# Optimization experiments

Hardware: AMD Instinct MI355X
Metric: run time of the kernel (lower is better)

The kernel has to match this reference:

```python
import jax, jax.numpy as jnp
import numpy as np

HEADS = 8
LN_EPS = 1e-5


def _elu_plus_one(t):
    # F.elu(x) + 1 == exp(x) for x<0, x+1 for x>=0
    return jax.nn.elu(t) + 1.0


def setup_inputs() -> dict:
    key = jax.random.key(0)
    k1, k2, k3 = jax.random.split(key, 3)
    dim = 256
    x = jax.random.normal(k1, (16, dim, 64, 64), dtype=jnp.float32)
    w_qkv = jax.random.normal(k2, (3 * dim, dim), dtype=jnp.float32) * 0.02
    w_out = jax.random.normal(k3, (dim, dim), dtype=jnp.float32) * 0.02
    ln_gamma = jnp.ones((dim,), dtype=jnp.float32)
    ln_beta = jnp.zeros((dim,), dtype=jnp.float32)
    return {"x": x, "w_qkv": w_qkv, "w_out": w_out, "ln_gamma": ln_gamma, "ln_beta": ln_beta}


def reference(x, w_qkv, w_out, ln_gamma, ln_beta):
    b, c, h, w = x.shape
    hd = c // HEADS
    n = h * w
    # 1x1 conv == per-pixel matmul over channels
    qkv = jnp.einsum('bchw,oc->bohw', x, w_qkv)  # [b, 3c, h, w]
    q, k, v = jnp.split(qkv, 3, axis=1)
    q = q.reshape(b, HEADS, hd, n)
    k = k.reshape(b, HEADS, hd, n)
    v = v.reshape(b, HEADS, hd, n)
    qk = _elu_plus_one(q)
    kk = _elu_plus_one(k)
    # channel-wise kv reduction over spatial positions (NOT an outer product)
    kv = jnp.sum(kk * v, axis=-1, keepdims=True)        # [b, heads, hd, 1]
    denom = jnp.maximum(jnp.sum(kk, axis=-1, keepdims=True), 1e-6)
    out = qk * (kv / denom)                              # [b, heads, hd, n]
    out = out.reshape(b, c, h, w)
    out = jnp.einsum('bchw,oc->bohw', out, w_out)        # 1x1 output conv
    # LayerNorm over channel dim (module permutes to NHWC first)
    t = jnp.transpose(out, (0, 2, 3, 1))                 # [b, h, w, c]
    mu = jnp.mean(t, axis=-1, keepdims=True)
    var = jnp.mean(jnp.square(t - mu), axis=-1, keepdims=True)
    t = (t - mu) * jax.lax.rsqrt(var + LN_EPS) * ln_gamma + ln_beta
    return jnp.transpose(t, (0, 3, 1, 2))
```

## Files before the change

kernel.cpp:

```cpp
#include <hip/hip_runtime.h>


#define NB 16
#define NC 256
#define NN 4096
#define LN_EPS 1e-5f
#define IOSCALE (1.0f/1024.0f)

typedef _Float16 f16;
typedef _Float16 f16x8 __attribute__((ext_vector_type(8)));
typedef _Float16 f16x4v __attribute__((ext_vector_type(4)));
typedef float f32x4 __attribute__((ext_vector_type(4)));

typedef __attribute__((address_space(1))) const unsigned int* as1cu32;
typedef __attribute__((address_space(3))) unsigned int* as3u32;

__device__ __forceinline__ void gload16(const void* g, void* l) {
  __builtin_amdgcn_global_load_lds((as1cu32)g, (as3u32)l, 16, 0, 0);
}
__device__ __forceinline__ float elu1(float x) {
  return x > 0.f ? x + 1.f : __expf(x);
}
#define MFMA16 __builtin_amdgcn_mfma_f32_16x16x32_f16

__global__ __launch_bounds__(256) void k_init(const float* __restrict__ wqkv,
                                              const float* __restrict__ wout,
                                              f16* __restrict__ wh,
                                              f16* __restrict__ wouth,
                                              float* __restrict__ kvden) {
  int i = blockIdx.x * 256 + threadIdx.x;
  wh[i] = (f16)wqkv[i];
  if (i < 65536) wouth[i] = (f16)wout[i];
  if (i < 8192) kvden[i] = 0.f;
}

__global__ __launch_bounds__(256) void k_transpose(const float* __restrict__ x,
                                                   f16* __restrict__ xh) {
  __shared__ float t[64 * 65];
  const int b = blockIdx.z, c0 = blockIdx.y * 64, n0 = blockIdx.x * 64;
  const int tid = threadIdx.x;
#pragma unroll
  for (int i = 0; i < 4; ++i) {
    int lin = tid + i * 256;
    int r = lin >> 4;
    int cg = lin & 15;
    const float4 v = *reinterpret_cast<const float4*>(
        &x[((size_t)(b * NC + c0 + r)) * NN + n0 + cg * 4]);
    t[r * 65 + cg * 4 + 0] = v.x;
    t[r * 65 + cg * 4 + 1] = v.y;
    t[r * 65 + cg * 4 + 2] = v.z;
    t[r * 65 + cg * 4 + 3] = v.w;
  }
  __syncthreads();
#pragma unroll
  for (int i = 0; i < 4; ++i) {
    int lin = tid + i * 256;
    int nr = lin >> 4;
    int cg = lin & 15;
    f16x4v h;
    h[0] = (f16)t[(cg * 4 + 0) * 65 + nr];
    h[1] = (f16)t[(cg * 4 + 1) * 65 + nr];
    h[2] = (f16)t[(cg * 4 + 2) * 65 + nr];
    h[3] = (f16)t[(cg * 4 + 3) * 65 + nr];
    *reinterpret_cast<f16x4v*>(&xh[((size_t)(b * NN + n0 + nr)) * NC + c0 + cg * 4]) = h;
  }
}

__global__ __launch_bounds__(512, 4) void k_kv(const f16* __restrict__ xh,
                                               const f16* __restrict__ wh,
                                               float* __restrict__ kv,
                                               float* __restrict__ den) {
  __shared__ __align__(16) f16 Xc[2][64 * 32];
  __shared__ __align__(16) f16 Bt[2][512 * 32];
  const int b = blockIdx.y;
  const int n0 = blockIdx.x * 64;
  const int tid = threadIdx.x;
  const int lane = tid & 63;
  const int wv = tid >> 6;
  const int ng = wv >> 2, cg = wv & 3;
  const int l15 = lane & 15, lg = lane >> 4;
  const int srow = lane >> 2;
  const int scol = (((lane & 3) ^ (srow & 3)) * 8);
  const int xu = ((lg ^ (l15 & 3)) << 3);

  f32x4 kacc[2][4] = {};
  f32x4 vacc[2][4] = {};

#pragma unroll
  for (int i = 0; i < 4; ++i) {
    const int inst = wv * 4 + i;
    gload16(wh + (size_t)(256 + inst * 16 + srow) * NC + scol, &Bt[0][inst * 512]);
  }
  if (wv < 4)
    gload16(xh + ((size_t)(b * NN + n0 + wv * 16 + srow)) * NC + scol, &Xc[0][wv * 512]);
  __syncthreads();

  for (int s = 0; s < 8; ++s) {
    const int cb = s & 1, nb = (s + 1) & 1;
    if (s < 7) {
      const int c0 = (s + 1) * 32;
#pragma unroll
      for (int i = 0; i < 4; ++i) {
        const int inst = wv * 4 + i;
        gload16(wh + (size_t)(256 + inst * 16 + srow) * NC + c0 + scol, &Bt[nb][inst * 512]);
      }
      if (wv < 4)
        gload16(xh + ((size_t)(b * NN + n0 + wv * 16 + srow)) * NC + c0 + scol, &Xc[nb][wv * 512]);
    }
    const f16x8 a0 = *(const f16x8*)(&Xc[cb][(ng * 32 + l15) * 32 + xu]);
    const f16x8 a1 = *(const f16x8*)(&Xc[cb][(ng * 32 + 16 + l15) * 32 + xu]);
#pragma unroll
    for (int f = 0; f < 4; ++f) {
      const f16x8 bk = *(const f16x8*)(&Bt[cb][(cg * 64 + f * 16 + l15) * 32 + xu]);
      kacc[0][f] = MFMA16(a0, bk, kacc[0][f], 0, 0, 0);
      kacc[1][f] = MFMA16(a1, bk, kacc[1][f], 0, 0, 0);
      const f16x8 bv = *(const f16x8*)(&Bt[cb][(256 + cg * 64 + f * 16 + l15) * 32 + xu]);
      vacc[0][f] = MFMA16(a0, bv, vacc[0][f], 0, 0, 0);
      vacc[1][f] = MFMA16(a1, bv, vacc[1][f], 0, 0, 0);
    }
    if (s < 7) __syncthreads();
  }

  float pkv[4] = {0.f, 0.f, 0.f, 0.f}, pden[4] = {0.f, 0.f, 0.f, 0.f};
#pragma unroll
  for (int f = 0; f < 4; ++f)
#pragma unroll
    for (int m = 0; m < 2; ++m)
#pragma unroll
      for (int j = 0; j < 4; ++j) {
        const float kk = elu1(kacc[m][f][j]);
        pkv[f] += kk * vacc[m][f][j];
        pden[f] += kk;
      }
#pragma unroll
  for (int f = 0; f < 4; ++f) {
    pkv[f] += __shfl_xor(pkv[f], 16, 64);
    pkv[f] += __shfl_xor(pkv[f], 32, 64);
    pden[f] += __shfl_xor(pden[f], 16, 64);
    pden[f] += __shfl_xor(pden[f], 32, 64);
  }
  if (lane < 16) {
#pragma unroll
    for (int f = 0; f < 4; ++f) {
      const int c = cg * 64 + f * 16 + lane;
      atomicAdd(&kv[b * NC + c], pkv[f]);
      atomicAdd(&den[b * NC + c], pden[f]);
    }
  }
}

__global__ __launch_bounds__(512, 4) void k_fused2(const f16* __restrict__ xh,
                                                   const f16* __restrict__ wh,
                                                   const f16* __restrict__ wouth,
                                                   const float* __restrict__ kv,
                                                   const float* __restrict__ den,
                                                   const float* __restrict__ gamma,
                                                   const float* __restrict__ beta,
                                                   float* __restrict__ out) {
  __shared__ __align__(16) f16 Xc[2][64 * 32];
  __shared__ __align__(16) f16 Wt[2][256 * 32];
  __shared__ __align__(16) f16 Q[64 * 256];
  const int b = blockIdx.y;
  const int n0 = blockIdx.x * 64;
  const int tid = threadIdx.x;
  const int lane = tid & 63;
  const int wv = tid >> 6;
  const int cg = wv >> 1, ng = wv & 1;
  const int l15 = lane & 15, lg = lane >> 4;
  const int srow = lane >> 2;
  const int scol = (((lane & 3) ^ (srow & 3)) * 8);
  const int xu = ((lg ^ (l15 & 3)) << 3);

  float sreg[4][4];
#pragma unroll
  for (int m = 0; m < 4; ++m)
#pragma unroll
    for (int j = 0; j < 4; ++j) {
      const int c = cg * 64 + m * 16 + lg * 4 + j;
      sreg[m][j] = kv[b * NC + c] / fmaxf(den[b * NC + c], 1e-6f) * 1024.0f;
    }

#pragma unroll
  for (int i = 0; i < 2; ++i) {
    const int inst = wv * 2 + i;
    gload16(wh + (size_t)(inst * 16 + srow) * NC + scol, &Wt[0][inst * 512]);
  }
  if (wv < 4)
    gload16(xh + ((size_t)(b * NN + n0 + wv * 16 + srow)) * NC + scol, &Xc[0][wv * 512]);
  __syncthreads();

  f32x4 acc[4][2] = {};
  for (int s = 0; s < 8; ++s) {
    const int cb = s & 1, nb = (s + 1) & 1;
    if (s < 7) {
      const int c0 = (s + 1) * 32;
#pragma unroll
      for (int i = 0; i < 2; ++i) {
        const int inst = wv * 2 + i;
        gload16(wh + (size_t)(inst * 16 + srow) * NC + c0 + scol, &Wt[nb][inst * 512]);
      }
      if (wv < 4)
        gload16(xh + ((size_t)(b * NN + n0 + wv * 16 + srow)) * NC + c0 + scol, &Xc[nb][wv * 512]);
    } else {
#pragma unroll
      for (int i = 0; i < 2; ++i) {
        const int inst = wv * 2 + i;
        gload16(wouth + (size_t)(inst * 16 + srow) * NC + scol, &Wt[nb][inst * 512]);
      }
    }
    f16x8 a[4], bx[2];
#pragma unroll
    for (int m = 0; m < 4; ++m)
      a[m] = *(const f16x8*)(&Wt[cb][(cg * 64 + m * 16 + l15) * 32 + xu]);
#pragma unroll
    for (int f = 0; f < 2; ++f)
      bx[f] = *(const f16x8*)(&Xc[cb][(ng * 32 + f * 16 + l15) * 32 + xu]);
#pragma unroll
    for (int m = 0; m < 4; ++m)
#pragma unroll
      for (int f = 0; f < 2; ++f)
        acc[m][f] = MFMA16(a[m], bx[f], acc[m][f], 0, 0, 0);
    if (s < 7) __syncthreads();
  }

#pragma unroll
  for (int m = 0; m < 4; ++m) {
#pragma unroll
    for (int f = 0; f < 2; ++f) {
      const int n = ng * 32 + f * 16 + l15;
      const int ch = cg * 64 + m * 16 + lg * 4;
      const int u = ch >> 3;
      f16x4v h;
#pragma unroll
      for (int j = 0; j < 4; ++j)
        h[j] = (f16)(elu1(acc[m][f][j]) * sreg[m][j]);
      *reinterpret_cast<f16x4v*>(&Q[n * 256 + ((u ^ (n & 7)) << 3) + (ch & 7)]) = h;
    }
  }
  __syncthreads();

  f32x4 acc2[4][2] = {};
  for (int s = 0; s < 8; ++s) {
    const int cb = s & 1, nb = (s + 1) & 1;
    if (s < 7) {
      const int c0 = (s + 1) * 32;
#pragma unroll
      for (int i = 0; i < 2; ++i) {
        const int inst = wv * 2 + i;
        gload16(wouth + (size_t)(inst * 16 + srow) * NC + c0 + scol, &Wt[nb][inst * 512]);
      }
    }
    f16x8 a[4], bq[2];
#pragma unroll
    for (int m = 0; m < 4; ++m)
      a[m] = *(const f16x8*)(&Wt[cb][(cg * 64 + m * 16 + l15) * 32 + xu]);
#pragma unroll
    for (int f = 0; f < 2; ++f) {
      const int n = ng * 32 + f * 16 + l15;
      const int U = s * 4 + lg;
      bq[f] = *(const f16x8*)(&Q[n * 256 + ((U ^ (n & 7)) << 3)]);
    }
#pragma unroll
    for (int m = 0; m < 4; ++m)
#pragma unroll
      for (int f = 0; f < 2; ++f)
        acc2[m][f] = MFMA16(a[m], bq[f], acc2[m][f], 0, 0, 0);
    if (s < 7) __syncthreads();
  }

  float* red1 = (float*)(&Xc[0][0]);
  float* red2 = red1 + 256;
  float* smu = red2 + 256;
  float* srs = smu + 64;
  float s1[2] = {0, 0}, s2[2] = {0, 0};
#pragma unroll
  for (int f = 0; f < 2; ++f)
#pragma unroll
    for (int m = 0; m < 4; ++m)
#pragma unroll
      for (int j = 0; j < 4; ++j) {
        const float v = acc2[m][f][j];
        s1[f] += v;
        s2[f] += v * v;
      }
#pragma unroll
  for (int f = 0; f < 2; ++f) {
    s1[f] += __shfl_xor(s1[f], 16, 64);
    s1[f] += __shfl_xor(s1[f], 32, 64);
    s2[f] += __shfl_xor(s2[f], 16, 64);
    s2[f] += __shfl_xor(s2[f], 32, 64);
  }
  __syncthreads();
  if (lane < 16) {
#pragma unroll
    for (int f = 0; f < 2; ++f) {
      red1[cg * 64 + ng * 32 + f * 16 + lane] = s1[f];
      red2[cg * 64 + ng * 32 + f * 16 + lane] = s2[f];
    }
  }
  __syncthreads();
  if (tid < 64) {
    const float a1 = red1[tid] + red1[64 + tid] + red1[128 + tid] + red1[192 + tid];
    const float a2 = red2[tid] + red2[64 + tid] + red2[128 + tid] + red2[192 + tid];
    const float mu = a1 * (IOSCALE / 256.f);
    const float e2 = a2 * (IOSCALE * IOSCALE / 256.f);
    smu[tid] = mu;
    srs[tid] = rsqrtf(e2 - mu * mu + LN_EPS);
  }
  __syncthreads();
#pragma unroll
  for (int m = 0; m < 4; ++m) {
    const int ob = cg * 64 + m * 16 + lg * 4;
#pragma unroll
    for (int j = 0; j < 4; ++j) {
      const int o = ob + j;
      const float g = gamma[o], be = beta[o];
#pragma unroll
      for (int f = 0; f < 2; ++f) {
        const int col = ng * 32 + f * 16 + l15;
        const float v = acc2[m][f][j] * IOSCALE;
        out[((size_t)(b * NC + o)) * NN + n0 + col] = (v - smu[col]) * srs[col] * g + be;
      }
    }
  }
}

extern "C" void kernel_launch(void* const* d_in, const int* in_sizes, int n_in,
                              void* d_out, int out_size, void* d_ws, size_t ws_size,
                              hipStream_t stream) {
  const float* x = (const float*)d_in[0];
  const float* w_qkv = (const float*)d_in[1];
  const float* w_out = (const float*)d_in[2];
  const float* ln_g = (const float*)d_in[3];
  const float* ln_b = (const float*)d_in[4];
  float* out = (float*)d_out;

  char* wsb = (char*)d_ws;
  const size_t OFF_WH = 0;
  const size_t OFF_WOUTH = 393216;
  const size_t OFF_XH = OFF_WOUTH + 131072;
  const size_t OFF_KV = OFF_XH + 33554432;
  const size_t OFF_DEN = OFF_KV + 16384;

  f16* wh = (f16*)(wsb + OFF_WH);
  f16* wouth = (f16*)(wsb + OFF_WOUTH);
  f16* xh = (f16*)(wsb + OFF_XH);
  float* kv = (float*)(wsb + OFF_KV);
  float* den = (float*)(wsb + OFF_DEN);

  k_init<<<768, 256, 0, stream>>>(w_qkv, w_out, wh, wouth, kv);
  k_transpose<<<dim3(64, 4, 16), 256, 0, stream>>>(x, xh);
  k_kv<<<dim3(64, 16), 512, 0, stream>>>(xh, wh, kv, den);
  k_fused2<<<dim3(64, 16), 512, 0, stream>>>(xh, wh, wouth, kv, den, ln_g, ln_b, out);
}
```

Baseline: 94.43 us.

## Triple-buffer fused kernel loads, double spatial tile, use raw barriers and waitcnts

Restructures k_fused2 so each block handles 128 spatial positions instead of 64, halving the grid and doubling per-wave MFMA work and weight reuse. Global-to-LDS staging moves from double to triple buffering, with manual vmcnt waits, raw s_barrier and setprio around the MFMA bursts, so loads overlap compute with fewer full syncs. The kv/den scale is computed once into shared memory. In exchange the kernel needs much more LDS and more registers, lowering occupancy to about one block per CU, and the manual waitcnt counting is fragile.

```diff
diff --git a/kernel.cpp b/kernel.cpp
--- a/kernel.cpp
+++ b/kernel.cpp
@@ -22,6 +22,25 @@
   return x > 0.f ? x + 1.f : __expf(x);
 }
 #define MFMA16 __builtin_amdgcn_mfma_f32_16x16x32_f16
+
+#define FENCE() asm volatile("" ::: "memory")
+#define SBAR()                                  \
+  do {                                          \
+    FENCE();                                    \
+    __builtin_amdgcn_sched_barrier(0);          \
+    __builtin_amdgcn_s_barrier();               \
+    __builtin_amdgcn_sched_barrier(0);          \
+    FENCE();                                    \
+  } while (0)
+
+template <int N> __device__ __forceinline__ void waitv() {
+  if constexpr (N == 0) asm volatile("s_waitcnt vmcnt(0)" ::: "memory");
+  else if constexpr (N == 2) asm volatile("s_waitcnt vmcnt(2)" ::: "memory");
+  else asm volatile("s_waitcnt vmcnt(3)" ::: "memory");
+}
+__device__ __forceinline__ void waitl0() {
+  asm volatile("s_waitcnt lgkmcnt(0)" ::: "memory");
+}
 
 __global__ __launch_bounds__(256) void k_init(const float* __restrict__ wqkv,
                                               const float* __restrict__ wout,
@@ -149,7 +168,7 @@
   }
 }
 
-__global__ __launch_bounds__(512, 4) void k_fused2(const f16* __restrict__ xh,
+__global__ __launch_bounds__(512, 1) void k_fused2(const f16* __restrict__ xh,
                                                    const f16* __restrict__ wh,
                                                    const f16* __restrict__ wouth,
                                                    const float* __restrict__ kv,
@@ -157,11 +176,12 @@
                                                    const float* __restrict__ gamma,
                                                    const float* __restrict__ beta,
                                                    float* __restrict__ out) {
-  __shared__ __align__(16) f16 Xc[2][64 * 32];
-  __shared__ __align__(16) f16 Wt[2][256 * 32];
-  __shared__ __align__(16) f16 Q[64 * 256];
+  __shared__ __align__(16) f16 Wt[3 * 256 * 32];
+  __shared__ __align__(16) f16 Xc[3 * 128 * 32];
+  __shared__ __align__(16) f16 Q[128 * 256];
+  __shared__ float s1024[256];
   const int b = blockIdx.y;
-  const int n0 = blockIdx.x * 64;
+  const int n0 = blockIdx.x * 128;
   const int tid = threadIdx.x;
   const int lane = tid & 63;
   const int wv = tid >> 6;
@@ -171,110 +191,114 @@
   const int scol = (((lane & 3) ^ (srow & 3)) * 8);
   const int xu = ((lg ^ (l15 & 3)) << 3);
 
-  float sreg[4][4];
-#pragma unroll
-  for (int m = 0; m < 4; ++m)
-#pragma unroll
-    for (int j = 0; j < 4; ++j) {
-      const int c = cg * 64 + m * 16 + lg * 4 + j;
-      sreg[m][j] = kv[b * NC + c] / fmaxf(den[b * NC + c], 1e-6f) * 1024.0f;
-    }
-
-#pragma unroll
-  for (int i = 0; i < 2; ++i) {
-    const int inst = wv * 2 + i;
-    gload16(wh + (size_t)(inst * 16 + srow) * NC + scol, &Wt[0][inst * 512]);
-  }
-  if (wv < 4)
-    gload16(xh + ((size_t)(b * NN + n0 + wv * 16 + srow)) * NC + scol, &Xc[0][wv * 512]);
-  __syncthreads();
-
-  f32x4 acc[4][2] = {};
+  if (tid < 256)
+    s1024[tid] = kv[b * NC + tid] / fmaxf(den[b * NC + tid], 1e-6f) * 1024.0f;
+  waitv<0>();
+
+  auto stageC = [&](int c, int buf) {
+    const int c0 = c * 32;
+    gload16(xh + ((size_t)(b * NN + n0 + wv * 16 + srow)) * NC + c0 + scol,
+            &Xc[buf * 4096 + wv * 512]);
+    gload16(wh + (size_t)(wv * 32 + srow) * NC + c0 + scol,
+            &Wt[buf * 8192 + wv * 1024]);
+    gload16(wh + (size_t)(wv * 32 + 16 + srow) * NC + c0 + scol,
+            &Wt[buf * 8192 + wv * 1024 + 512]);
+  };
+  auto stageW = [&](int c, int buf) {
+    const int c0 = c * 32;
+    gload16(wouth + (size_t)(wv * 32 + srow) * NC + c0 + scol,
+            &Wt[buf * 8192 + wv * 1024]);
+    gload16(wouth + (size_t)(wv * 32 + 16 + srow) * NC + c0 + scol,
+            &Wt[buf * 8192 + wv * 1024 + 512]);
+  };
+
+  stageC(0, 0);
+  stageC(1, 1);
+  waitv<3>();
+  waitl0();
+  SBAR();
+
+  f32x4 acc[4][4] = {};
   for (int s = 0; s < 8; ++s) {
-    const int cb = s & 1, nb = (s + 1) & 1;
-    if (s < 7) {
-      const int c0 = (s + 1) * 32;
-#pragma unroll
-      for (int i = 0; i < 2; ++i) {
-        const int inst = wv * 2 + i;
-        gload16(wh + (size_t)(inst * 16 + srow) * NC + c0 + scol, &Wt[nb][inst * 512]);
-      }
-      if (wv < 4)
-        gload16(xh + ((size_t)(b * NN + n0 + wv * 16 + srow)) * NC + c0 + scol, &Xc[nb][wv * 512]);
-    } else {
-#pragma unroll
-      for (int i = 0; i < 2; ++i) {
-        const int inst = wv * 2 + i;
-        gload16(wouth + (size_t)(inst * 16 + srow) * NC + scol, &Wt[nb][inst * 512]);
-      }
-    }
-    f16x8 a[4], bx[2];
-#pragma unroll
-    for (int m = 0; m < 4; ++m)
-      a[m] = *(const f16x8*)(&Wt[cb][(cg * 64 + m * 16 + l15) * 32 + xu]);
-#pragma unroll
-    for (int f = 0; f < 2; ++f)
-      bx[f] = *(const f16x8*)(&Xc[cb][(ng * 32 + f * 16 + l15) * 32 + xu]);
-#pragma unroll
-    for (int m = 0; m < 4; ++m)
-#pragma unroll
-      for (int f = 0; f < 2; ++f)
-        acc[m][f] = MFMA16(a[m], bx[f], acc[m][f], 0, 0, 0);
-    if (s < 7) __syncthreads();
+    if (s < 6) stageC(s + 2, (s + 2) % 3);
+    else stageW(s - 6, (s + 2) % 3);
+    {
+      const f16* Wb = &Wt[(s % 3) * 8192];
+      const f16* Xb = &Xc[(s % 3) * 4096];
+      f16x8 a[4], bx[4];
+#pragma unroll
+      for (int m = 0; m < 4; ++m)
+        a[m] = *(const f16x8*)(Wb + (cg * 64 + m * 16 + l15) * 32 + xu);
+#pragma unroll
+      for (int f = 0; f < 4; ++f)
+        bx[f] = *(const f16x8*)(Xb + (ng * 64 + f * 16 + l15) * 32 + xu);
+      __builtin_amdgcn_s_setprio(1);
+#pragma unroll
+      for (int m = 0; m < 4; ++m)
+#pragma unroll
+        for (int f = 0; f < 4; ++f)
+          acc[m][f] = MFMA16(a[m], bx[f], acc[m][f], 0, 0, 0);
+      __builtin_amdgcn_s_setprio(0);
+    }
+    if (s < 6) waitv<3>();
+    else waitv<2>();
+    SBAR();
   }
 
 #pragma unroll
   for (int m = 0; m < 4; ++m) {
-#pragma unroll
-    for (int f = 0; f < 2; ++f) {
-      const int n = ng * 32 + f * 16 + l15;
-      const int ch = cg * 64 + m * 16 + lg * 4;
-      const int u = ch >> 3;
+    const int ch = cg * 64 + m * 16 + lg * 4;
+    const float4 sv = *reinterpret_cast<const float4*>(&s1024[ch]);
+    const int u = ch >> 3;
+#pragma unroll
+    for (int f = 0; f < 4; ++f) {
+      const int n = ng * 64 + f * 16 + l15;
       f16x4v h;
-#pragma unroll
-      for (int j = 0; j < 4; ++j)
-        h[j] = (f16)(elu1(acc[m][f][j]) * sreg[m][j]);
+      h[0] = (f16)(elu1(acc[m][f][0]) * sv.x);
+      h[1] = (f16)(elu1(acc[m][f][1]) * sv.y);
+      h[2] = (f16)(elu1(acc[m][f][2]) * sv.z);
+      h[3] = (f16)(elu1(acc[m][f][3]) * sv.w);
       *reinterpret_cast<f16x4v*>(&Q[n * 256 + ((u ^ (n & 7)) << 3) + (ch & 7)]) = h;
     }
   }
-  __syncthreads();
-
-  f32x4 acc2[4][2] = {};
+  waitv<2>();
+  waitl0();
+  SBAR();
+
+  f32x4 acc2[4][4] = {};
   for (int s = 0; s < 8; ++s) {
-    const int cb = s & 1, nb = (s + 1) & 1;
-    if (s < 7) {
-      const int c0 = (s + 1) * 32;
-#pragma unroll
-      for (int i = 0; i < 2; ++i) {
-        const int inst = wv * 2 + i;
-        gload16(wouth + (size_t)(inst * 16 + srow) * NC + c0 + scol, &Wt[nb][inst * 512]);
-      }
-    }
-    f16x8 a[4], bq[2];
-#pragma unroll
-    for (int m = 0; m < 4; ++m)
-      a[m] = *(const f16x8*)(&Wt[cb][(cg * 64 + m * 16 + l15) * 32 + xu]);
-#pragma unroll
-    for (int f = 0; f < 2; ++f) {
-      const int n = ng * 32 + f * 16 + l15;
-      const int U = s * 4 + lg;
-      bq[f] = *(const f16x8*)(&Q[n * 256 + ((U ^ (n & 7)) << 3)]);
-    }
-#pragma unroll
-    for (int m = 0; m < 4; ++m)
-#pragma unroll
-      for (int f = 0; f < 2; ++f)
-        acc2[m][f] = MFMA16(a[m], bq[f], acc2[m][f], 0, 0, 0);
-    if (s < 7) __syncthreads();
-  }
-
-  float* red1 = (float*)(&Xc[0][0]);
-  float* red2 = red1 + 256;
-  float* smu = red2 + 256;
-  float* srs = smu + 64;
-  float s1[2] = {0, 0}, s2[2] = {0, 0};
-#pragma unroll
-  for (int f = 0; f < 2; ++f)
+    if (s < 6) stageW(s + 2, (s + 1) % 3);
+    {
+      const f16* Wb = &Wt[((s + 2) % 3) * 8192];
+      f16x8 a[4], bq[4];
+#pragma unroll
+      for (int m = 0; m < 4; ++m)
+        a[m] = *(const f16x8*)(Wb + (cg * 64 + m * 16 + l15) * 32 + xu);
+#pragma unroll
+      for (int f = 0; f < 4; ++f) {
+        const int n = ng * 64 + f * 16 + l15;
+        const int U = s * 4 + lg;
+        bq[f] = *(const f16x8*)(&Q[n * 256 + ((U ^ (n & 7)) << 3)]);
+      }
+      __builtin_amdgcn_s_setprio(1);
+#pragma unroll
+      for (int m = 0; m < 4; ++m)
+#pragma unroll
+        for (int f = 0; f < 4; ++f)
+          acc2[m][f] = MFMA16(a[m], bq[f], acc2[m][f], 0, 0, 0);
+      __builtin_amdgcn_s_setprio(0);
+    }
+    if (s < 6) { waitv<2>(); SBAR(); }
+    else if (s == 6) { waitv<0>(); SBAR(); }
+  }
+
+  float* red1 = (float*)(&Xc[0]);
+  float* red2 = red1 + 512;
+  float* smu = red2 + 512;
+  float* srs = smu + 128;
+  float s1[4] = {0, 0, 0, 0}, s2[4] = {0, 0, 0, 0};
+#pragma unroll
+  for (int f = 0; f < 4; ++f)
 #pragma unroll
     for (int m = 0; m < 4; ++m)
 #pragma unroll
@@ -284,7 +308,7 @@
         s2[f] += v * v;
       }
 #pragma unroll
-  for (int f = 0; f < 2; ++f) {
+  for (int f = 0; f < 4; ++f) {
     s1[f] += __shfl_xor(s1[f], 16, 64);
     s1[f] += __shfl_xor(s1[f], 32, 64);
     s2[f] += __shfl_xor(s2[f], 16, 64);
@@ -293,15 +317,16 @@
   __syncthreads();
   if (lane < 16) {
 #pragma unroll
-    for (int f = 0; f < 2; ++f) {
-      red1[cg * 64 + ng * 32 + f * 16 + lane] = s1[f];
-      red2[cg * 64 + ng * 32 + f * 16 + lane] = s2[f];
-    }
-  }
-  __syncthreads();
-  if (tid < 64) {
-    const float a1 = red1[tid] + red1[64 + tid] + red1[128 + tid] + red1[192 + tid];
-    const float a2 = red2[tid] + red2[64 + tid] + red2[128 + tid] + red2[192 + tid];
+    for (int f = 0; f < 4; ++f) {
+      const int col = ng * 64 + f * 16 + lane;
+      red1[cg * 128 + col] = s1[f];
+      red2[cg * 128 + col] = s2[f];
+    }
+  }
+  __syncthreads();
+  if (tid < 128) {
+    const float a1 = red1[tid] + red1[128 + tid] + red1[256 + tid] + red1[384 + tid];
+    const float a2 = red2[tid] + red2[128 + tid] + red2[256 + tid] + red2[384 + tid];
     const float mu = a1 * (IOSCALE / 256.f);
     const float e2 = a2 * (IOSCALE * IOSCALE / 256.f);
     smu[tid] = mu;
@@ -316,8 +341,8 @@
       const int o = ob + j;
       const float g = gamma[o], be = beta[o];
 #pragma unroll
-      for (int f = 0; f < 2; ++f) {
-        const int col = ng * 32 + f * 16 + l15;
+      for (int f = 0; f < 4; ++f) {
+        const int col = ng * 64 + f * 16 + l15;
         const float v = acc2[m][f][j] * IOSCALE;
         out[((size_t)(b * NC + o)) * NN + n0 + col] = (v - smu[col]) * srs[col] * g + be;
       }
@@ -351,5 +376,5 @@
   k_init<<<768, 256, 0, stream>>>(w_qkv, w_out, wh, wouth, kv);
   k_transpose<<<dim3(64, 4, 16), 256, 0, stream>>>(x, xh);
   k_kv<<<dim3(64, 16), 512, 0, stream>>>(xh, wh, kv, den);
-  k_fused2<<<dim3(64, 16), 512, 0, stream>>>(xh, wh, wouth, kv, den, ln_g, ln_b, out);
-}
+  k_fused2<<<dim3(32, 16), 512, 0, stream>>>(xh, wh, wouth, kv, den, ln_g, ln_b, out);
+}
```

Result: no change. 94.67 us (+0.3%).

## Stage full X tile in padded LDS and stream weights directly from global

Applied to the files above, without the earlier changes.

Both k_kv and k_fused2 now load the whole 64x256 activation tile into a padded LDS buffer once, then read weight fragments straight from global memory (through cache) into registers instead of double-buffering weight slices through LDS with async global_load_lds. k_kv changes its wave decomposition so that weights are the A operand and pixels the B operand. Its reduction becomes a per-row shuffle across 16 lanes, followed by atomics from more lanes. k_fused2 reuses the X buffer to hold the Q intermediate and drops most per-stage barriers. The intent is to cut synchronisation and LDS traffic, at the cost of exposed global-load latency for weights in the inner loop.

```diff
diff --git a/kernel.cpp b/kernel.cpp
--- a/kernel.cpp
+++ b/kernel.cpp
@@ -12,12 +12,6 @@
 typedef _Float16 f16x4v __attribute__((ext_vector_type(4)));
 typedef float f32x4 __attribute__((ext_vector_type(4)));
 
-typedef __attribute__((address_space(1))) const unsigned int* as1cu32;
-typedef __attribute__((address_space(3))) unsigned int* as3u32;
-
-__device__ __forceinline__ void gload16(const void* g, void* l) {
-  __builtin_amdgcn_global_load_lds((as1cu32)g, (as3u32)l, 16, 0, 0);
-}
 __device__ __forceinline__ float elu1(float x) {
   return x > 0.f ? x + 1.f : __expf(x);
 }
@@ -70,81 +64,67 @@
                                                const f16* __restrict__ wh,
                                                float* __restrict__ kv,
                                                float* __restrict__ den) {
-  __shared__ __align__(16) f16 Xc[2][64 * 32];
-  __shared__ __align__(16) f16 Bt[2][512 * 32];
+  __shared__ __align__(16) f16 Xt[64 * 264];
   const int b = blockIdx.y;
   const int n0 = blockIdx.x * 64;
   const int tid = threadIdx.x;
   const int lane = tid & 63;
   const int wv = tid >> 6;
-  const int ng = wv >> 2, cg = wv & 3;
+  const int cg = wv >> 1, ng = wv & 1;
   const int l15 = lane & 15, lg = lane >> 4;
-  const int srow = lane >> 2;
-  const int scol = (((lane & 3) ^ (srow & 3)) * 8);
-  const int xu = ((lg ^ (l15 & 3)) << 3);
-
-  f32x4 kacc[2][4] = {};
-  f32x4 vacc[2][4] = {};
 
 #pragma unroll
   for (int i = 0; i < 4; ++i) {
-    const int inst = wv * 4 + i;
-    gload16(wh + (size_t)(256 + inst * 16 + srow) * NC + scol, &Bt[0][inst * 512]);
-  }
-  if (wv < 4)
-    gload16(xh + ((size_t)(b * NN + n0 + wv * 16 + srow)) * NC + scol, &Xc[0][wv * 512]);
-  __syncthreads();
-
+    const int idx = i * 512 + tid;
+    const int row = idx >> 5, u = idx & 31;
+    const f16x8 h = *(const f16x8*)(xh + ((size_t)(b * NN + n0 + row)) * NC + u * 8);
+    *reinterpret_cast<f16x8*>(&Xt[row * 264 + u * 8]) = h;
+  }
+  __syncthreads();
+
+  f32x4 kacc[4][2] = {};
+  f32x4 vacc[4][2] = {};
+  const f16* wk = wh + (size_t)(256 + cg * 64 + l15) * NC;
+  const f16* wvp = wh + (size_t)(512 + cg * 64 + l15) * NC;
+#pragma unroll
   for (int s = 0; s < 8; ++s) {
-    const int cb = s & 1, nb = (s + 1) & 1;
-    if (s < 7) {
-      const int c0 = (s + 1) * 32;
-#pragma unroll
-      for (int i = 0; i < 4; ++i) {
-        const int inst = wv * 4 + i;
-        gload16(wh + (size_t)(256 + inst * 16 + srow) * NC + c0 + scol, &Bt[nb][inst * 512]);
-      }
-      if (wv < 4)
-        gload16(xh + ((size_t)(b * NN + n0 + wv * 16 + srow)) * NC + c0 + scol, &Xc[nb][wv * 512]);
-    }
-    const f16x8 a0 = *(const f16x8*)(&Xc[cb][(ng * 32 + l15) * 32 + xu]);
-    const f16x8 a1 = *(const f16x8*)(&Xc[cb][(ng * 32 + 16 + l15) * 32 + xu]);
-#pragma unroll
-    for (int f = 0; f < 4; ++f) {
-      const f16x8 bk = *(const f16x8*)(&Bt[cb][(cg * 64 + f * 16 + l15) * 32 + xu]);
-      kacc[0][f] = MFMA16(a0, bk, kacc[0][f], 0, 0, 0);
-      kacc[1][f] = MFMA16(a1, bk, kacc[1][f], 0, 0, 0);
-      const f16x8 bv = *(const f16x8*)(&Bt[cb][(256 + cg * 64 + f * 16 + l15) * 32 + xu]);
-      vacc[0][f] = MFMA16(a0, bv, vacc[0][f], 0, 0, 0);
-      vacc[1][f] = MFMA16(a1, bv, vacc[1][f], 0, 0, 0);
-    }
-    if (s < 7) __syncthreads();
-  }
-
-  float pkv[4] = {0.f, 0.f, 0.f, 0.f}, pden[4] = {0.f, 0.f, 0.f, 0.f};
-#pragma unroll
-  for (int f = 0; f < 4; ++f)
-#pragma unroll
-    for (int m = 0; m < 2; ++m)
-#pragma unroll
-      for (int j = 0; j < 4; ++j) {
+    const int k0 = s * 32 + lg * 8;
+    f16x8 bx[2];
+#pragma unroll
+    for (int f = 0; f < 2; ++f)
+      bx[f] = *(const f16x8*)(&Xt[(ng * 32 + f * 16 + l15) * 264 + k0]);
+#pragma unroll
+    for (int m = 0; m < 4; ++m) {
+      const f16x8 ak = *(const f16x8*)(wk + (size_t)(m * 16) * NC + k0);
+      const f16x8 av = *(const f16x8*)(wvp + (size_t)(m * 16) * NC + k0);
+#pragma unroll
+      for (int f = 0; f < 2; ++f) {
+        kacc[m][f] = MFMA16(ak, bx[f], kacc[m][f], 0, 0, 0);
+        vacc[m][f] = MFMA16(av, bx[f], vacc[m][f], 0, 0, 0);
+      }
+    }
+  }
+
+#pragma unroll
+  for (int m = 0; m < 4; ++m) {
+#pragma unroll
+    for (int j = 0; j < 4; ++j) {
+      float a = 0.f, d = 0.f;
+#pragma unroll
+      for (int f = 0; f < 2; ++f) {
         const float kk = elu1(kacc[m][f][j]);
-        pkv[f] += kk * vacc[m][f][j];
-        pden[f] += kk;
-      }
-#pragma unroll
-  for (int f = 0; f < 4; ++f) {
-    pkv[f] += __shfl_xor(pkv[f], 16, 64);
-    pkv[f] += __shfl_xor(pkv[f], 32, 64);
-    pden[f] += __shfl_xor(pden[f], 16, 64);
-    pden[f] += __shfl_xor(pden[f], 32, 64);
-  }
-  if (lane < 16) {
-#pragma unroll
-    for (int f = 0; f < 4; ++f) {
-      const int c = cg * 64 + f * 16 + lane;
-      atomicAdd(&kv[b * NC + c], pkv[f]);
-      atomicAdd(&den[b * NC + c], pden[f]);
+        a += kk * vacc[m][f][j];
+        d += kk;
+      }
+      a += __shfl_xor(a, 1, 64);  d += __shfl_xor(d, 1, 64);
+      a += __shfl_xor(a, 2, 64);  d += __shfl_xor(d, 2, 64);
+      a += __shfl_xor(a, 4, 64);  d += __shfl_xor(d, 4, 64);
+      a += __shfl_xor(a, 8, 64);  d += __shfl_xor(d, 8, 64);
+      if (l15 == 0) {
+        const int c = cg * 64 + m * 16 + lg * 4 + j;
+        atomicAdd(&kv[b * NC + c], a);
+        atomicAdd(&den[b * NC + c], d);
+      }
     }
   }
 }
@@ -157,9 +137,9 @@
                                                    const float* __restrict__ gamma,
                                                    const float* __restrict__ beta,
                                                    float* __restrict__ out) {
-  __shared__ __align__(16) f16 Xc[2][64 * 32];
-  __shared__ __align__(16) f16 Wt[2][256 * 32];
-  __shared__ __align__(16) f16 Q[64 * 256];
+  __shared__ __align__(16) f16 XQ[64 * 264];
+  __shared__ float s1024[256];
+  __shared__ float red1[4][64], red2[4][64], smu[64], srs[64];
   const int b = blockIdx.y;
   const int n0 = blockIdx.x * 64;
   const int tid = threadIdx.x;
@@ -167,111 +147,76 @@
   const int wv = tid >> 6;
   const int cg = wv >> 1, ng = wv & 1;
   const int l15 = lane & 15, lg = lane >> 4;
-  const int srow = lane >> 2;
-  const int scol = (((lane & 3) ^ (srow & 3)) * 8);
-  const int xu = ((lg ^ (l15 & 3)) << 3);
-
-  float sreg[4][4];
-#pragma unroll
-  for (int m = 0; m < 4; ++m)
-#pragma unroll
-    for (int j = 0; j < 4; ++j) {
-      const int c = cg * 64 + m * 16 + lg * 4 + j;
-      sreg[m][j] = kv[b * NC + c] / fmaxf(den[b * NC + c], 1e-6f) * 1024.0f;
-    }
-
-#pragma unroll
-  for (int i = 0; i < 2; ++i) {
-    const int inst = wv * 2 + i;
-    gload16(wh + (size_t)(inst * 16 + srow) * NC + scol, &Wt[0][inst * 512]);
-  }
-  if (wv < 4)
-    gload16(xh + ((size_t)(b * NN + n0 + wv * 16 + srow)) * NC + scol, &Xc[0][wv * 512]);
+
+#pragma unroll
+  for (int i = 0; i < 4; ++i) {
+    const int idx = i * 512 + tid;
+    const int row = idx >> 5, u = idx & 31;
+    const f16x8 h = *(const f16x8*)(xh + ((size_t)(b * NN + n0 + row)) * NC + u * 8);
+    *reinterpret_cast<f16x8*>(&XQ[row * 264 + u * 8]) = h;
+  }
+  if (tid < 256)
+    s1024[tid] = kv[b * NC + tid] / fmaxf(den[b * NC + tid], 1e-6f) * 1024.0f;
   __syncthreads();
 
   f32x4 acc[4][2] = {};
-  for (int s = 0; s < 8; ++s) {
-    const int cb = s & 1, nb = (s + 1) & 1;
-    if (s < 7) {
-      const int c0 = (s + 1) * 32;
-#pragma unroll
-      for (int i = 0; i < 2; ++i) {
-        const int inst = wv * 2 + i;
-        gload16(wh + (size_t)(inst * 16 + srow) * NC + c0 + scol, &Wt[nb][inst * 512]);
-      }
-      if (wv < 4)
-        gload16(xh + ((size_t)(b * NN + n0 + wv * 16 + srow)) * NC + c0 + scol, &Xc[nb][wv * 512]);
-    } else {
-#pragma unroll
-      for (int i = 0; i < 2; ++i) {
-        const int inst = wv * 2 + i;
-        gload16(wouth + (size_t)(inst * 16 + srow) * NC + scol, &Wt[nb][inst * 512]);
-      }
-    }
-    f16x8 a[4], bx[2];
-#pragma unroll
-    for (int m = 0; m < 4; ++m)
-      a[m] = *(const f16x8*)(&Wt[cb][(cg * 64 + m * 16 + l15) * 32 + xu]);
-#pragma unroll
-    for (int f = 0; f < 2; ++f)
-      bx[f] = *(const f16x8*)(&Xc[cb][(ng * 32 + f * 16 + l15) * 32 + xu]);
-#pragma unroll
-    for (int m = 0; m < 4; ++m)
+  {
+    const f16* wq = wh + (size_t)(cg * 64 + l15) * NC;
+#pragma unroll
+    for (int s = 0; s < 8; ++s) {
+      const int k0 = s * 32 + lg * 8;
+      f16x8 bx[2];
 #pragma unroll
       for (int f = 0; f < 2; ++f)
-        acc[m][f] = MFMA16(a[m], bx[f], acc[m][f], 0, 0, 0);
-    if (s < 7) __syncthreads();
-  }
+        bx[f] = *(const f16x8*)(&XQ[(ng * 32 + f * 16 + l15) * 264 + k0]);
+#pragma unroll
+      for (int m = 0; m < 4; ++m) {
+        const f16x8 aq = *(const f16x8*)(wq + (size_t)(m * 16) * NC + k0);
+#pragma unroll
+        for (int f = 0; f < 2; ++f)
+          acc[m][f] = MFMA16(aq, bx[f], acc[m][f], 0, 0, 0);
+      }
+    }
+  }
+  __syncthreads();
 
 #pragma unroll
   for (int m = 0; m < 4; ++m) {
+    const int ch = cg * 64 + m * 16 + lg * 4;
+    const float4 sv = *reinterpret_cast<const float4*>(&s1024[ch]);
 #pragma unroll
     for (int f = 0; f < 2; ++f) {
       const int n = ng * 32 + f * 16 + l15;
-      const int ch = cg * 64 + m * 16 + lg * 4;
-      const int u = ch >> 3;
       f16x4v h;
-#pragma unroll
-      for (int j = 0; j < 4; ++j)
-        h[j] = (f16)(elu1(acc[m][f][j]) * sreg[m][j]);
-      *reinterpret_cast<f16x4v*>(&Q[n * 256 + ((u ^ (n & 7)) << 3) + (ch & 7)]) = h;
+      h[0] = (f16)(elu1(acc[m][f][0]) * sv.x);
+      h[1] = (f16)(elu1(acc[m][f][1]) * sv.y);
+      h[2] = (f16)(elu1(acc[m][f][2]) * sv.z);
+      h[3] = (f16)(elu1(acc[m][f][3]) * sv.w);
+      *reinterpret_cast<f16x4v*>(&XQ[n * 264 + ch]) = h;
     }
   }
   __syncthreads();
 
   f32x4 acc2[4][2] = {};
-  for (int s = 0; s < 8; ++s) {
-    const int cb = s & 1, nb = (s + 1) & 1;
-    if (s < 7) {
-      const int c0 = (s + 1) * 32;
-#pragma unroll
-      for (int i = 0; i < 2; ++i) {
-        const int inst = wv * 2 + i;
-        gload16(wouth + (size_t)(inst * 16 + srow) * NC + c0 + scol, &Wt[nb][inst * 512]);
-      }
-    }
-    f16x8 a[4], bq[2];
-#pragma unroll
-    for (int m = 0; m < 4; ++m)
-      a[m] = *(const f16x8*)(&Wt[cb][(cg * 64 + m * 16 + l15) * 32 + xu]);
-#pragma unroll
-    for (int f = 0; f < 2; ++f) {
-      const int n = ng * 32 + f * 16 + l15;
-      const int U = s * 4 + lg;
-      bq[f] = *(const f16x8*)(&Q[n * 256 + ((U ^ (n & 7)) << 3)]);
-    }
-#pragma unroll
-    for (int m = 0; m < 4; ++m)
+  {
+    const f16* wo = wouth + (size_t)(cg * 64 + l15) * NC;
+#pragma unroll
+    for (int s = 0; s < 8; ++s) {
+      const int k0 = s * 32 + lg * 8;
+      f16x8 bq[2];
 #pragma unroll
       for (int f = 0; f < 2; ++f)
-        acc2[m][f] = MFMA16(a[m], bq[f], acc2[m][f], 0, 0, 0);
-    if (s < 7) __syncthreads();
-  }
-
-  float* red1 = (float*)(&Xc[0][0]);
-  float* red2 = red1 + 256;
-  float* smu = red2 + 256;
-  float* srs = smu + 64;
+        bq[f] = *(const f16x8*)(&XQ[(ng * 32 + f * 16 + l15) * 264 + k0]);
+#pragma unroll
+      for (int m = 0; m < 4; ++m) {
+        const f16x8 ao = *(const f16x8*)(wo + (size_t)(m * 16) * NC + k0);
+#pragma unroll
+        for (int f = 0; f < 2; ++f)
+          acc2[m][f] = MFMA16(ao, bq[f], acc2[m][f], 0, 0, 0);
+      }
+    }
+  }
+
   float s1[2] = {0, 0}, s2[2] = {0, 0};
 #pragma unroll
   for (int f = 0; f < 2; ++f)
@@ -290,18 +235,18 @@
     s2[f] += __shfl_xor(s2[f], 16, 64);
     s2[f] += __shfl_xor(s2[f], 32, 64);
   }
-  __syncthreads();
   if (lane < 16) {
 #pragma unroll
     for (int f = 0; f < 2; ++f) {
-      red1[cg * 64 + ng * 32 + f * 16 + lane] = s1[f];
-      red2[cg * 64 + ng * 32 + f * 16 + lane] = s2[f];
+      const int col = ng * 32 + f * 16 + lane;
+      red1[cg][col] = s1[f];
+      red2[cg][col] = s2[f];
     }
   }
   __syncthreads();
   if (tid < 64) {
-    const float a1 = red1[tid] + red1[64 + tid] + red1[128 + tid] + red1[192 + tid];
-    const float a2 = red2[tid] + red2[64 + tid] + red2[128 + tid] + red2[192 + tid];
+    const float a1 = red1[0][tid] + red1[1][tid] + red1[2][tid] + red1[3][tid];
+    const float a2 = red2[0][tid] + red2[1][tid] + red2[2][tid] + red2[3][tid];
     const float mu = a1 * (IOSCALE / 256.f);
     const float e2 = a2 * (IOSCALE * IOSCALE / 256.f);
     smu[tid] = mu;
```

New measurement: 190.0 us. 101% more time.

## Double spatial tile to 128 and stage full X tile in LDS once

Applied to the files above, without the earlier changes.

Both the kv and fused kernels now process 128 spatial positions per 1024-thread block instead of 64 with 512 threads. The whole X tile (128x256 fp16) is loaded into LDS up front instead of being double-buffered per K-step. Only the weight slices stay double-buffered, and the fused kernel reuses the X buffer to hold Q. The goal is to halve how often each block re-reads the weights and to cut per-step global loads. In exchange LDS per block grows to about 96KB, which limits blocks per CU, and the grid is halved to 512 blocks.

```diff
diff --git a/kernel.cpp b/kernel.cpp
--- a/kernel.cpp
+++ b/kernel.cpp
@@ -66,57 +66,71 @@
   }
 }
 
-__global__ __launch_bounds__(512, 4) void k_kv(const f16* __restrict__ xh,
-                                               const f16* __restrict__ wh,
-                                               float* __restrict__ kv,
-                                               float* __restrict__ den) {
-  __shared__ __align__(16) f16 Xc[2][64 * 32];
+__global__ __launch_bounds__(1024, 4) void k_kv(const f16* __restrict__ xh,
+                                                const f16* __restrict__ wh,
+                                                float* __restrict__ kv,
+                                                float* __restrict__ den) {
+  __shared__ __align__(16) f16 Xt[128 * 256];
   __shared__ __align__(16) f16 Bt[2][512 * 32];
   const int b = blockIdx.y;
-  const int n0 = blockIdx.x * 64;
+  const int n0 = blockIdx.x * 128;
   const int tid = threadIdx.x;
   const int lane = tid & 63;
   const int wv = tid >> 6;
   const int ng = wv >> 2, cg = wv & 3;
   const int l15 = lane & 15, lg = lane >> 4;
-  const int srow = lane >> 2;
-  const int scol = (((lane & 3) ^ (srow & 3)) * 8);
-  const int xu = ((lg ^ (l15 & 3)) << 3);
+
+  {
+    const int rsub = lane >> 5;
+    const int u = lane & 31;
+#pragma unroll
+    for (int i = 0; i < 4; ++i) {
+      const int inst = wv * 4 + i;
+      const int row = inst * 2 + rsub;
+      gload16(xh + ((size_t)(b * NN + n0 + row)) * NC + ((u ^ (row & 31)) * 8),
+              &Xt[inst * 512]);
+    }
+  }
+
+  auto stageB = [&](int s, int bb) {
+    const int c0 = s * 32;
+    const int rsub = lane >> 2;
+    const int u = lane & 3;
+#pragma unroll
+    for (int i = 0; i < 2; ++i) {
+      const int inst = wv * 2 + i;
+      const int row = inst * 16 + rsub;
+      gload16(wh + (size_t)(256 + row) * NC + c0 + ((u ^ ((row >> 1) & 3)) * 8),
+              &Bt[bb][inst * 512]);
+    }
+  };
+
+  stageB(0, 0);
+  __syncthreads();
 
   f32x4 kacc[2][4] = {};
   f32x4 vacc[2][4] = {};
-
-#pragma unroll
-  for (int i = 0; i < 4; ++i) {
-    const int inst = wv * 4 + i;
-    gload16(wh + (size_t)(256 + inst * 16 + srow) * NC + scol, &Bt[0][inst * 512]);
-  }
-  if (wv < 4)
-    gload16(xh + ((size_t)(b * NN + n0 + wv * 16 + srow)) * NC + scol, &Xc[0][wv * 512]);
-  __syncthreads();
-
   for (int s = 0; s < 8; ++s) {
-    const int cb = s & 1, nb = (s + 1) & 1;
-    if (s < 7) {
-      const int c0 = (s + 1) * 32;
-#pragma unroll
-      for (int i = 0; i < 4; ++i) {
-        const int inst = wv * 4 + i;
-        gload16(wh + (size_t)(256 + inst * 16 + srow) * NC + c0 + scol, &Bt[nb][inst * 512]);
+    const int cb = s & 1;
+    if (s < 7) stageB(s + 1, cb ^ 1);
+    f16x8 a[2];
+#pragma unroll
+    for (int m = 0; m < 2; ++m) {
+      const int R = ng * 32 + m * 16 + l15;
+      const int U = s * 4 + lg;
+      a[m] = *(const f16x8*)(&Xt[R * 256 + ((U ^ (R & 31)) * 8)]);
+    }
+#pragma unroll
+    for (int f = 0; f < 4; ++f) {
+      const int Rk = cg * 64 + f * 16 + l15;
+      const f16x8 bk = *(const f16x8*)(&Bt[cb][Rk * 32 + ((lg ^ ((Rk >> 1) & 3)) * 8)]);
+      const int Rv = 256 + Rk;
+      const f16x8 bv = *(const f16x8*)(&Bt[cb][Rv * 32 + ((lg ^ ((Rv >> 1) & 3)) * 8)]);
+#pragma unroll
+      for (int m = 0; m < 2; ++m) {
+        kacc[m][f] = MFMA16(a[m], bk, kacc[m][f], 0, 0, 0);
+        vacc[m][f] = MFMA16(a[m], bv, vacc[m][f], 0, 0, 0);
       }
-      if (wv < 4)
-        gload16(xh + ((size_t)(b * NN + n0 + wv * 16 + srow)) * NC + c0 + scol, &Xc[nb][wv * 512]);
-    }
-    const f16x8 a0 = *(const f16x8*)(&Xc[cb][(ng * 32 + l15) * 32 + xu]);
-    const f16x8 a1 = *(const f16x8*)(&Xc[cb][(ng * 32 + 16 + l15) * 32 + xu]);
-#pragma unroll
-    for (int f = 0; f < 4; ++f) {
-      const f16x8 bk = *(const f16x8*)(&Bt[cb][(cg * 64 + f * 16 + l15) * 32 + xu]);
-      kacc[0][f] = MFMA16(a0, bk, kacc[0][f], 0, 0, 0);
-      kacc[1][f] = MFMA16(a1, bk, kacc[1][f], 0, 0, 0);
-      const f16x8 bv = *(const f16x8*)(&Bt[cb][(256 + cg * 64 + f * 16 + l15) * 32 + xu]);
-      vacc[0][f] = MFMA16(a0, bv, vacc[0][f], 0, 0, 0);
-      vacc[1][f] = MFMA16(a1, bv, vacc[1][f], 0, 0, 0);
     }
     if (s < 7) __syncthreads();
   }
@@ -149,116 +163,108 @@
   }
 }
 
-__global__ __launch_bounds__(512, 4) void k_fused2(const f16* __restrict__ xh,
-                                                   const f16* __restrict__ wh,
-                                                   const f16* __restrict__ wouth,
-                                                   const float* __restrict__ kv,
-                                                   const float* __restrict__ den,
-                                                   const float* __restrict__ gamma,
-                                                   const float* __restrict__ beta,
-                                                   float* __restrict__ out) {
-  __shared__ __align__(16) f16 Xc[2][64 * 32];
+__global__ __launch_bounds__(1024, 4) void k_fused2(const f16* __restrict__ xh,
+                                                    const f16* __restrict__ wh,
+                                                    const f16* __restrict__ wouth,
+                                                    const float* __restrict__ kv,
+                                                    const float* __restrict__ den,
+                                                    const float* __restrict__ gamma,
+                                                    const float* __restrict__ beta,
+                                                    float* __restrict__ out) {
+  __shared__ __align__(16) f16 XQ[128 * 256];
   __shared__ __align__(16) f16 Wt[2][256 * 32];
-  __shared__ __align__(16) f16 Q[64 * 256];
+  __shared__ float s1024[256];
   const int b = blockIdx.y;
-  const int n0 = blockIdx.x * 64;
+  const int n0 = blockIdx.x * 128;
   const int tid = threadIdx.x;
   const int lane = tid & 63;
   const int wv = tid >> 6;
-  const int cg = wv >> 1, ng = wv & 1;
+  const int cg = wv & 3, ng = wv >> 2;
   const int l15 = lane & 15, lg = lane >> 4;
-  const int srow = lane >> 2;
-  const int scol = (((lane & 3) ^ (srow & 3)) * 8);
-  const int xu = ((lg ^ (l15 & 3)) << 3);
-
-  float sreg[4][4];
-#pragma unroll
-  for (int m = 0; m < 4; ++m)
-#pragma unroll
-    for (int j = 0; j < 4; ++j) {
-      const int c = cg * 64 + m * 16 + lg * 4 + j;
-      sreg[m][j] = kv[b * NC + c] / fmaxf(den[b * NC + c], 1e-6f) * 1024.0f;
-    }
-
-#pragma unroll
-  for (int i = 0; i < 2; ++i) {
-    const int inst = wv * 2 + i;
-    gload16(wh + (size_t)(inst * 16 + srow) * NC + scol, &Wt[0][inst * 512]);
-  }
-  if (wv < 4)
-    gload16(xh + ((size_t)(b * NN + n0 + wv * 16 + srow)) * NC + scol, &Xc[0][wv * 512]);
+
+  {
+    const int rsub = lane >> 5;
+    const int u = lane & 31;
+#pragma unroll
+    for (int i = 0; i < 4; ++i) {
+      const int inst = wv * 4 + i;
+      const int row = inst * 2 + rsub;
+      gload16(xh + ((size_t)(b * NN + n0 + row)) * NC + ((u ^ (row & 31)) * 8),
+              &XQ[inst * 512]);
+    }
+  }
+  if (tid < 256)
+    s1024[tid] = kv[b * NC + tid] / fmaxf(den[b * NC + tid], 1e-6f) * 1024.0f;
+
+  auto stageW = [&](const f16* __restrict__ W, int s, int bb) {
+    const int c0 = s * 32;
+    const int row = wv * 16 + (lane >> 2);
+    const int u = lane & 3;
+    gload16(W + (size_t)row * NC + c0 + ((u ^ ((row >> 1) & 3)) * 8),
+            &Wt[bb][wv * 512]);
+  };
+
+  stageW(wh, 0, 0);
   __syncthreads();
 
   f32x4 acc[4][2] = {};
   for (int s = 0; s < 8; ++s) {
-    const int cb = s & 1, nb = (s + 1) & 1;
-    if (s < 7) {
-      const int c0 = (s + 1) * 32;
-#pragma unroll
-      for (int i = 0; i < 2; ++i) {
-        const int inst = wv * 2 + i;
-        gload16(wh + (size_t)(inst * 16 + srow) * NC + c0 + scol, &Wt[nb][inst * 512]);
-      }
-      if (wv < 4)
-        gload16(xh + ((size_t)(b * NN + n0 + wv * 16 + srow)) * NC + c0 + scol, &Xc[nb][wv * 512]);
-    } else {
-#pragma unroll
-      for (int i = 0; i < 2; ++i) {
-        const int inst = wv * 2 + i;
-        gload16(wouth + (size_t)(inst * 16 + srow) * NC + scol, &Wt[nb][inst * 512]);
-      }
-    }
+    const int cb = s & 1;
+    if (s < 7) stageW(wh, s + 1, cb ^ 1);
+    else stageW(wouth, 0, cb ^ 1);
     f16x8 a[4], bx[2];
 #pragma unroll
-    for (int m = 0; m < 4; ++m)
-      a[m] = *(const f16x8*)(&Wt[cb][(cg * 64 + m * 16 + l15) * 32 + xu]);
-#pragma unroll
-    for (int f = 0; f < 2; ++f)
-      bx[f] = *(const f16x8*)(&Xc[cb][(ng * 32 + f * 16 + l15) * 32 + xu]);
+    for (int m = 0; m < 4; ++m) {
+      const int R = cg * 64 + m * 16 + l15;
+      a[m] = *(const f16x8*)(&Wt[cb][R * 32 + ((lg ^ ((R >> 1) & 3)) * 8)]);
+    }
+#pragma unroll
+    for (int f = 0; f < 2; ++f) {
+      const int Rn = ng * 32 + f * 16 + l15;
+      const int U = s * 4 + lg;
+      bx[f] = *(const f16x8*)(&XQ[Rn * 256 + ((U ^ (Rn & 31)) * 8)]);
+    }
 #pragma unroll
     for (int m = 0; m < 4; ++m)
 #pragma unroll
       for (int f = 0; f < 2; ++f)
         acc[m][f] = MFMA16(a[m], bx[f], acc[m][f], 0, 0, 0);
-    if (s < 7) __syncthreads();
+    __syncthreads();
   }
 
 #pragma unroll
   for (int m = 0; m < 4; ++m) {
+    const int ch = cg * 64 + m * 16 + lg * 4;
+    const float4 sv = *reinterpret_cast<const float4*>(&s1024[ch]);
+    const int u = ch >> 3;
 #pragma unroll
     for (int f = 0; f < 2; ++f) {
       const int n = ng * 32 + f * 16 + l15;
-      const int ch = cg * 64 + m * 16 + lg * 4;
-      const int u = ch >> 3;
       f16x4v h;
-#pragma unroll
-      for (int j = 0; j < 4; ++j)
-        h[j] = (f16)(elu1(acc[m][f][j]) * sreg[m][j]);
-      *reinterpret_cast<f16x4v*>(&Q[n * 256 + ((u ^ (n & 7)) << 3) + (ch & 7)]) = h;
+      h[0] = (f16)(elu1(acc[m][f][0]) * sv.x);
+      h[1] = (f16)(elu1(acc[m][f][1]) * sv.y);
+      h[2] = (f16)(elu1(acc[m][f][2]) * sv.z);
+      h[3] = (f16)(elu1(acc[m][f][3]) * sv.w);
+      *reinterpret_cast<f16x4v*>(&XQ[n * 256 + ((u ^ (n & 31)) * 8) + (ch & 7)]) = h;
     }
   }
   __syncthreads();
 
   f32x4 acc2[4][2] = {};
   for (int s = 0; s < 8; ++s) {
-    const int cb = s & 1, nb = (s + 1) & 1;
-    if (s < 7) {
-      const int c0 = (s + 1) * 32;
-#pragma unroll
-      for (int i = 0; i < 2; ++i) {
-        const int inst = wv * 2 + i;
-        gload16(wouth + (size_t)(inst * 16 + srow) * NC + c0 + scol, &Wt[nb][inst * 512]);
-      }
-    }
+    const int cb = s & 1;
+    if (s < 7) stageW(wouth, s + 1, cb ^ 1);
     f16x8 a[4], bq[2];
 #pragma unroll
-    for (int m = 0; m < 4; ++m)
-      a[m] = *(const f16x8*)(&Wt[cb][(cg * 64 + m * 16 + l15) * 32 + xu]);
+    for (int m = 0; m < 4; ++m) {
+      const int R = cg * 64 + m * 16 + l15;
+      a[m] = *(const f16x8*)(&Wt[cb][R * 32 + ((lg ^ ((R >> 1) & 3)) * 8)]);
+    }
 #pragma unroll
     for (int f = 0; f < 2; ++f) {
       const int n = ng * 32 + f * 16 + l15;
       const int U = s * 4 + lg;
-      bq[f] = *(const f16x8*)(&Q[n * 256 + ((U ^ (n & 7)) << 3)]);
+      bq[f] = *(const f16x8*)(&XQ[n * 256 + ((U ^ (n & 31)) * 8)]);
     }
 #pragma unroll
     for (int m = 0; m < 4; ++m)
@@ -268,10 +274,10 @@
     if (s < 7) __syncthreads();
   }
 
-  float* red1 = (float*)(&Xc[0][0]);
-  float* red2 = red1 + 256;
-  float* smu = red2 + 256;
-  float* srs = smu + 64;
+  float* red1 = (float*)(&Wt[0][0]);
+  float* red2 = red1 + 512;
+  float* smu = red2 + 512;
+  float* srs = smu + 128;
   float s1[2] = {0, 0}, s2[2] = {0, 0};
 #pragma unroll
   for (int f = 0; f < 2; ++f)
@@ -294,14 +300,15 @@
   if (lane < 16) {
 #pragma unroll
     for (int f = 0; f < 2; ++f) {
-      red1[cg * 64 + ng * 32 + f * 16 + lane] = s1[f];
-      red2[cg * 64 + ng * 32 + f * 16 + lane] = s2[f];
-    }
-  }
-  __syncthreads();
-  if (tid < 64) {
-    const float a1 = red1[tid] + red1[64 + tid] + red1[128 + tid] + red1[192 + tid];
-    const float a2 = red2[tid] + red2[64 + tid] + red2[128 + tid] + red2[192 + tid];
+      const int col = ng * 32 + f * 16 + lane;
+      red1[cg * 128 + col] = s1[f];
+      red2[cg * 128 + col] = s2[f];
+    }
+  }
+  __syncthreads();
+  if (tid < 128) {
+    const float a1 = red1[tid] + red1[128 + tid] + red1[256 + tid] + red1[384 + tid];
+    const float a2 = red2[tid] + red2[128 + tid] + red2[256 + tid] + red2[384 + tid];
     const float mu = a1 * (IOSCALE / 256.f);
     const float e2 = a2 * (IOSCALE * IOSCALE / 256.f);
     smu[tid] = mu;
@@ -350,6 +357,6 @@
 
   k_init<<<768, 256, 0, stream>>>(w_qkv, w_out, wh, wouth, kv);
   k_transpose<<<dim3(64, 4, 16), 256, 0, stream>>>(x, xh);
-  k_kv<<<dim3(64, 16), 512, 0, stream>>>(xh, wh, kv, den);
-  k_fused2<<<dim3(64, 16), 512, 0, stream>>>(xh, wh, wouth, kv, den, ln_g, ln_b, out);
-}
+  k_kv<<<dim3(32, 16), 1024, 0, stream>>>(xh, wh, kv, den);
+  k_fused2<<<dim3(32, 16), 1024, 0, stream>>>(xh, wh, wouth, kv, den, ln_g, ln_b, out);
+}
```

Result: faster. 87.76 us (-7.1%).
